# Kernel optimization log

Measured on AMD Instinct MI355X. Metric: run time of the kernel, lower is better.

The kernel has to match this reference:

```python
import jax, jax.numpy as jnp
import numpy as np

B, M, N, C = 8, 4096, 4096, 3


def setup_inputs() -> dict:
    key = jax.random.key(0)
    k1, k2 = jax.random.split(key)
    set1 = jax.random.normal(k1, (B, M, C), dtype=jnp.float32)
    set2 = jax.random.normal(k2, (B, N, C), dtype=jnp.float32)
    return {"set1": set1, "set2": set2}


def _pairwise_dist(set1, set2):
    # ||a - b|| computed via expansion to avoid a (B,M,N,C) broadcast tensor.
    sq1 = jnp.sum(set1 * set1, axis=-1)  # (B, M)
    sq2 = jnp.sum(set2 * set2, axis=-1)  # (B, N)
    inner = jnp.einsum("bmc,bnc->bmn", set1, set2)  # (B, M, N)
    d2 = sq1[:, :, None] + sq2[:, None, :] - 2.0 * inner
    return jnp.sqrt(jnp.maximum(d2, 0.0))  # (B, M, N)


def reference(set1, set2):
    # Average (Chamfer-style) Hausdorff: mean of directed nearest-neighbor
    # distances in both directions, summed.  Output shape (B,).
    d = _pairwise_dist(set1, set2)                # (B, M, N)
    term_1 = jnp.mean(jnp.min(d, axis=2), axis=1)  # set1 -> set2
    term_2 = jnp.mean(jnp.min(d, axis=1), axis=1)  # set2 -> set1
    res = term_1 + term_2
    if res.shape[0] == 1:
        res = jnp.squeeze(res, axis=0)
    return res
```

## Files before the change

### kernel.cpp

```cpp
#include <hip/hip_runtime.h>
#include <hip/hip_bf16.h>
#include <math.h>

constexpr int NB   = 8;
constexpr int NPTS = 4096;
constexpr int NSEG = 4;
constexpr int NN   = NPTS / NSEG;

typedef __attribute__((ext_vector_type(8)))  short  short8;
typedef __attribute__((ext_vector_type(16))) float  f32x16;

__device__ inline unsigned short f2bf(float v) {
    __hip_bfloat16 t = __float2bfloat16(v);
    return *reinterpret_cast<unsigned short*>(&t);
}
__device__ inline float bf2f(unsigned short u) {
    __hip_bfloat16 t = *reinterpret_cast<__hip_bfloat16*>(&u);
    return __bfloat162float(t);
}

__global__ __launch_bounds__(256, 4) void mfma_min_kernel(
    const float* __restrict__ s1, const float* __restrict__ s2,
    float* __restrict__ pmin)
{
    __shared__ short8 blds[2048];

    int bid  = blockIdx.x;
    int nseg = bid & 3;
    int qb   = (bid >> 2) & 15;
    int g    = bid >> 6;
    int b    = g & 7, dir = g >> 3;

    const float* Q    = dir ? s2 : s1;
    const float* Tset = dir ? s1 : s2;

    int tid = threadIdx.x;
    int wid = tid >> 6, l = tid & 63;
    int c = l & 31, h = l >> 5;

    const float* tsrc = Tset + ((size_t)b * NPTS + (size_t)nseg * NN) * 3;
    #pragma unroll
    for (int k = 0; k < 4; ++k) {
        int p = k * 256 + tid;
        float x = tsrc[p*3+0], y = tsrc[p*3+1], z = tsrc[p*3+2];
        float sq = fmaf(z, z, fmaf(y, y, x * x));
        float tx = -2.0f*x, ty = -2.0f*y, tz = -2.0f*z;
        unsigned short thx = f2bf(tx), thy = f2bf(ty), thz = f2bf(tz);
        unsigned short tlx = f2bf(tx - bf2f(thx));
        unsigned short tly = f2bf(ty - bf2f(thy));
        unsigned short tlz = f2bf(tz - bf2f(thz));
        unsigned short sqh = f2bf(sq);
        unsigned short sql = f2bf(sq - bf2f(sqh));
        short8 tLo = {(short)thx,(short)thy,(short)thz,(short)thx,(short)thy,(short)thz,(short)sqh,(short)sql};
        short8 tHi = {(short)tlx,(short)tly,(short)tlz,0,0,0,0,0};
        int slot = (p >> 5) * 64 + (p & 31);
        blds[slot]      = tLo;
        blds[slot + 32] = tHi;
    }

    short8 qfr[2];
    #pragma unroll
    for (int f = 0; f < 2; ++f) {
        int qidx = qb * 256 + wid * 64 + f * 32 + c;
        const float* qp = Q + ((size_t)b * NPTS + qidx) * 3;
        float x = qp[0], y = qp[1], z = qp[2];
        unsigned short ahx = f2bf(x), ahy = f2bf(y), ahz = f2bf(z);
        if (h == 0) {
            unsigned short alx = f2bf(x - bf2f(ahx));
            unsigned short aly = f2bf(y - bf2f(ahy));
            unsigned short alz = f2bf(z - bf2f(ahz));
            unsigned short one = 0x3F80;
            qfr[f] = short8{(short)ahx,(short)ahy,(short)ahz,
                            (short)alx,(short)aly,(short)alz,(short)one,(short)one};
        } else {
            qfr[f] = short8{(short)ahx,(short)ahy,(short)ahz,0,0,0,0,0};
        }
    }
    __syncthreads();

    f32x16 zero, acc0, acc1;
    #pragma unroll
    for (int r = 0; r < 16; ++r) { zero[r] = 0.0f; acc0[r] = 3.4e38f; acc1[r] = 3.4e38f; }

    #pragma unroll 2
    for (int ntp = 0; ntp < 16; ++ntp) {
        short8 t0 = blds[(2*ntp  ) * 64 + l];
        short8 t1 = blds[(2*ntp+1) * 64 + l];
        f32x16 d0 = __builtin_amdgcn_mfma_f32_32x32x16_bf16(t0, qfr[0], zero, 0, 0, 0);
        f32x16 d1 = __builtin_amdgcn_mfma_f32_32x32x16_bf16(t1, qfr[0], zero, 0, 0, 0);
        #pragma unroll
        for (int r = 0; r < 16; ++r)
            acc0[r] = fminf(fminf(acc0[r], d0[r]), d1[r]);
        f32x16 e0 = __builtin_amdgcn_mfma_f32_32x32x16_bf16(t0, qfr[1], zero, 0, 0, 0);
        f32x16 e1 = __builtin_amdgcn_mfma_f32_32x32x16_bf16(t1, qfr[1], zero, 0, 0, 0);
        #pragma unroll
        for (int r = 0; r < 16; ++r)
            acc1[r] = fminf(fminf(acc1[r], e0[r]), e1[r]);
    }

    float* pg = pmin + ((size_t)g * NSEG + nseg) * NPTS;
    #pragma unroll
    for (int f = 0; f < 2; ++f) {
        f32x16& a = f ? acc1 : acc0;
        float v = a[0];
        #pragma unroll
        for (int r = 1; r < 16; ++r) v = fminf(v, a[r]);
        v = fminf(v, __shfl_xor(v, 32, 64));
        if (h == 0)
            pg[qb * 256 + wid * 64 + f * 32 + c] = v;
    }
}

__global__ __launch_bounds__(1024) void reduce_kernel(
    const float* __restrict__ s1, const float* __restrict__ s2,
    const float* __restrict__ pmin, float* __restrict__ out)
{
    int b = blockIdx.x;
    int t = threadIdx.x;

    float sum = 0.0f;
    #pragma unroll
    for (int dir = 0; dir < 2; ++dir) {
        int g = dir * NB + b;
        const float4* pg = reinterpret_cast<const float4*>(pmin + (size_t)g * NSEG * NPTS);
        float4 m = pg[t];
        #pragma unroll
        for (int s = 1; s < NSEG; ++s) {
            float4 v = pg[(size_t)s * 1024 + t];
            m.x = fminf(m.x, v.x); m.y = fminf(m.y, v.y);
            m.z = fminf(m.z, v.z); m.w = fminf(m.w, v.w);
        }
        const float* q = (dir ? s2 : s1) + ((size_t)b * NPTS + (size_t)4 * t) * 3;
        const float4* q4 = reinterpret_cast<const float4*>(q);
        float4 f0 = q4[0], f1 = q4[1], f2 = q4[2];
        float sa0 = fmaf(f0.z, f0.z, fmaf(f0.y, f0.y, f0.x * f0.x));
        float sa1 = fmaf(f1.y, f1.y, fmaf(f1.x, f1.x, f0.w * f0.w));
        float sa2 = fmaf(f2.x, f2.x, fmaf(f1.w, f1.w, f1.z * f1.z));
        float sa3 = fmaf(f2.w, f2.w, fmaf(f2.z, f2.z, f2.y * f2.y));
        sum += sqrtf(fmaxf(sa0 + m.x, 0.0f)) + sqrtf(fmaxf(sa1 + m.y, 0.0f))
             + sqrtf(fmaxf(sa2 + m.z, 0.0f)) + sqrtf(fmaxf(sa3 + m.w, 0.0f));
    }

    for (int off = 32; off > 0; off >>= 1)
        sum += __shfl_down(sum, off, 64);

    __shared__ float red[16];
    if ((t & 63) == 0) red[t >> 6] = sum;
    __syncthreads();
    if (t == 0) {
        float tt = 0.0f;
        #pragma unroll
        for (int w = 0; w < 16; ++w) tt += red[w];
        out[b] = tt * (1.0f / (float)NPTS);
    }
}

extern "C" void kernel_launch(void* const* d_in, const int* in_sizes, int n_in,
                              void* d_out, int out_size, void* d_ws, size_t ws_size,
                              hipStream_t stream) {
    const float* set1 = (const float*)d_in[0];
    const float* set2 = (const float*)d_in[1];
    float* out  = (float*)d_out;
    float* pmin = (float*)d_ws;

    mfma_min_kernel<<<16 * 16 * NSEG, 256, 0, stream>>>(set1, set2, pmin);
    reduce_kernel<<<NB, 1024, 0, stream>>>(set1, set2, pmin, out);
}
```

Before: 18.32 us.

## Drop target segmentation and fuse sqrt/mean reduction into MFMA kernel

Each block now loads the full 4096-point target set into LDS (128 KB) instead of a quarter, so grid shrinks from 1024 to 256 blocks. The full minimum is then available in-block, so the sqrt and per-block sum are computed there and only 256 partials are written, replaced by a tiny final kernel. This removes the partial-min workspace round trip and the heavy reduce kernel, but cuts parallelism to one block per CU with large LDS use and a 4x longer serial loop per block.

```diff
diff --git a/kernel.cpp b/kernel.cpp
--- a/kernel.cpp
+++ b/kernel.cpp
@@ -4,8 +4,7 @@
 
 constexpr int NB   = 8;
 constexpr int NPTS = 4096;
-constexpr int NSEG = 4;
-constexpr int NN   = NPTS / NSEG;
+constexpr int TPB  = 256;
 
 typedef __attribute__((ext_vector_type(8)))  short  short8;
 typedef __attribute__((ext_vector_type(16))) float  f32x16;
@@ -19,29 +18,28 @@
     return __bfloat162float(t);
 }
 
-__global__ __launch_bounds__(256, 4) void mfma_min_kernel(
+__global__ __launch_bounds__(TPB) void hausdorff_mfma_kernel(
     const float* __restrict__ s1, const float* __restrict__ s2,
-    float* __restrict__ pmin)
+    float* __restrict__ partial)
 {
-    __shared__ short8 blds[2048];
+    __shared__ short8 blds[2 * NPTS];
 
-    int bid  = blockIdx.x;
-    int nseg = bid & 3;
-    int qb   = (bid >> 2) & 15;
-    int g    = bid >> 6;
-    int b    = g & 7, dir = g >> 3;
+    int bid = blockIdx.x;
+    int qb  = bid & 15;
+    int g   = bid >> 4;
+    int b   = g & 7, dir = g >> 3;
 
-    const float* Q    = dir ? s2 : s1;
-    const float* Tset = dir ? s1 : s2;
+    const float* Q = dir ? s2 : s1;
+    const float* T = dir ? s1 : s2;
 
     int tid = threadIdx.x;
     int wid = tid >> 6, l = tid & 63;
     int c = l & 31, h = l >> 5;
 
-    const float* tsrc = Tset + ((size_t)b * NPTS + (size_t)nseg * NN) * 3;
-    #pragma unroll
-    for (int k = 0; k < 4; ++k) {
-        int p = k * 256 + tid;
+    const float* tsrc = T + (size_t)b * NPTS * 3;
+    #pragma unroll 4
+    for (int k = 0; k < 16; ++k) {
+        int p = k * TPB + tid;
         float x = tsrc[p*3+0], y = tsrc[p*3+1], z = tsrc[p*3+2];
         float sq = fmaf(z, z, fmaf(y, y, x * x));
         float tx = -2.0f*x, ty = -2.0f*y, tz = -2.0f*z;
@@ -58,12 +56,13 @@
         blds[slot + 32] = tHi;
     }
 
-    short8 qfr[2];
+    short8 qfr[2]; float qx[2], qy[2], qz[2];
     #pragma unroll
     for (int f = 0; f < 2; ++f) {
         int qidx = qb * 256 + wid * 64 + f * 32 + c;
         const float* qp = Q + ((size_t)b * NPTS + qidx) * 3;
         float x = qp[0], y = qp[1], z = qp[2];
+        qx[f] = x; qy[f] = y; qz[f] = z;
         unsigned short ahx = f2bf(x), ahy = f2bf(y), ahz = f2bf(z);
         if (h == 0) {
             unsigned short alx = f2bf(x - bf2f(ahx));
@@ -83,9 +82,9 @@
     for (int r = 0; r < 16; ++r) { zero[r] = 0.0f; acc0[r] = 3.4e38f; acc1[r] = 3.4e38f; }
 
     #pragma unroll 2
-    for (int ntp = 0; ntp < 16; ++ntp) {
-        short8 t0 = blds[(2*ntp  ) * 64 + l];
-        short8 t1 = blds[(2*ntp+1) * 64 + l];
+    for (int i = 0; i < 64; ++i) {
+        short8 t0 = blds[(2*i  ) * 64 + l];
+        short8 t1 = blds[(2*i+1) * 64 + l];
         f32x16 d0 = __builtin_amdgcn_mfma_f32_32x32x16_bf16(t0, qfr[0], zero, 0, 0, 0);
         f32x16 d1 = __builtin_amdgcn_mfma_f32_32x32x16_bf16(t1, qfr[0], zero, 0, 0, 0);
         #pragma unroll
@@ -98,7 +97,7 @@
             acc1[r] = fminf(fminf(acc1[r], e0[r]), e1[r]);
     }
 
-    float* pg = pmin + ((size_t)g * NSEG + nseg) * NPTS;
+    float s = 0.0f;
     #pragma unroll
     for (int f = 0; f < 2; ++f) {
         f32x16& a = f ? acc1 : acc0;
@@ -106,53 +105,34 @@
         #pragma unroll
         for (int r = 1; r < 16; ++r) v = fminf(v, a[r]);
         v = fminf(v, __shfl_xor(v, 32, 64));
-        if (h == 0)
-            pg[qb * 256 + wid * 64 + f * 32 + c] = v;
+        float sa = fmaf(qz[f], qz[f], fmaf(qy[f], qy[f], qx[f] * qx[f]));
+        s += sqrtf(fmaxf(sa + v, 0.0f));
     }
+    if (h) s = 0.0f;
+    for (int off = 32; off > 0; off >>= 1)
+        s += __shfl_down(s, off, 64);
+
+    __syncthreads();
+    float* red = reinterpret_cast<float*>(blds);
+    if (l == 0) red[wid] = s;
+    __syncthreads();
+    if (tid == 0)
+        partial[bid] = red[0] + red[1] + red[2] + red[3];
 }
 
-__global__ __launch_bounds__(1024) void reduce_kernel(
-    const float* __restrict__ s1, const float* __restrict__ s2,
-    const float* __restrict__ pmin, float* __restrict__ out)
+__global__ __launch_bounds__(64) void final_kernel(
+    const float* __restrict__ partial, float* __restrict__ out)
 {
-    int b = blockIdx.x;
-    int t = threadIdx.x;
-
-    float sum = 0.0f;
-    #pragma unroll
-    for (int dir = 0; dir < 2; ++dir) {
-        int g = dir * NB + b;
-        const float4* pg = reinterpret_cast<const float4*>(pmin + (size_t)g * NSEG * NPTS);
-        float4 m = pg[t];
+    int l = threadIdx.x;
+    float s = 0.0f;
+    if (l < 16) {
         #pragma unroll
-        for (int s = 1; s < NSEG; ++s) {
-            float4 v = pg[(size_t)s * 1024 + t];
-            m.x = fminf(m.x, v.x); m.y = fminf(m.y, v.y);
-            m.z = fminf(m.z, v.z); m.w = fminf(m.w, v.w);
-        }
-        const float* q = (dir ? s2 : s1) + ((size_t)b * NPTS + (size_t)4 * t) * 3;
-        const float4* q4 = reinterpret_cast<const float4*>(q);
-        float4 f0 = q4[0], f1 = q4[1], f2 = q4[2];
-        float sa0 = fmaf(f0.z, f0.z, fmaf(f0.y, f0.y, f0.x * f0.x));
-        float sa1 = fmaf(f1.y, f1.y, fmaf(f1.x, f1.x, f0.w * f0.w));
-        float sa2 = fmaf(f2.x, f2.x, fmaf(f1.w, f1.w, f1.z * f1.z));
-        float sa3 = fmaf(f2.w, f2.w, fmaf(f2.z, f2.z, f2.y * f2.y));
-        sum += sqrtf(fmaxf(sa0 + m.x, 0.0f)) + sqrtf(fmaxf(sa1 + m.y, 0.0f))
-             + sqrtf(fmaxf(sa2 + m.z, 0.0f)) + sqrtf(fmaxf(sa3 + m.w, 0.0f));
+        for (int j = 0; j < 16; ++j)
+            s += partial[l * 16 + j];
     }
-
-    for (int off = 32; off > 0; off >>= 1)
-        sum += __shfl_down(sum, off, 64);
-
-    __shared__ float red[16];
-    if ((t & 63) == 0) red[t >> 6] = sum;
-    __syncthreads();
-    if (t == 0) {
-        float tt = 0.0f;
-        #pragma unroll
-        for (int w = 0; w < 16; ++w) tt += red[w];
-        out[b] = tt * (1.0f / (float)NPTS);
-    }
+    float other = __shfl(s, l + 8, 64);
+    if (l < NB)
+        out[l] = (s + other) * (1.0f / (float)NPTS);
 }
 
 extern "C" void kernel_launch(void* const* d_in, const int* in_sizes, int n_in,
@@ -160,9 +140,9 @@
                               hipStream_t stream) {
     const float* set1 = (const float*)d_in[0];
     const float* set2 = (const float*)d_in[1];
-    float* out  = (float*)d_out;
-    float* pmin = (float*)d_ws;
+    float* out     = (float*)d_out;
+    float* partial = (float*)d_ws;
 
-    mfma_min_kernel<<<16 * 16 * NSEG, 256, 0, stream>>>(set1, set2, pmin);
-    reduce_kernel<<<NB, 1024, 0, stream>>>(set1, set2, pmin, out);
+    hausdorff_mfma_kernel<<<256, TPB, 0, stream>>>(set1, set2, partial);
+    final_kernel<<<1, 64, 0, stream>>>(partial, out);
 }
```

After: 26.83 us. 46.4% more time.
